# Performance work log

Measured on AMD Instinct MI355X. Metric: run time of the kernel, lower is better.

The kernel has to match this reference:

```python
import jax, jax.numpy as jnp
import numpy as np

N_NODES = 50000
N_EDGES = 600000  # incidence entries; hyperedge ids also live in [0, N_NODES)
HID = 128


def _prelu(x, a):
    return jnp.where(x >= 0, x, a * x)


def _hypergraph_conv(x, W, b, node_idx, edge_idx, num_nodes, num_hedges):
    # PyG HypergraphConv (use_attention=False, heads=1):
    # out = D^{-1} H B^{-1} H^T (X Theta) + bias
    xw = x @ W  # [N, F]
    ones = jnp.ones(node_idx.shape[0], dtype=x.dtype)
    D = jax.ops.segment_sum(ones, node_idx, num_segments=num_nodes)   # node degree
    B = jax.ops.segment_sum(ones, edge_idx, num_segments=num_hedges)  # hyperedge degree
    Dinv = jnp.where(D > 0, 1.0 / D, 0.0)
    Binv = jnp.where(B > 0, 1.0 / B, 0.0)
    # node -> hyperedge aggregation, scaled by B^{-1}
    m = jax.ops.segment_sum(xw[node_idx], edge_idx, num_segments=num_hedges) * Binv[:, None]
    # hyperedge -> node aggregation, scaled by D^{-1}
    out = jax.ops.segment_sum(m[edge_idx], node_idx, num_segments=num_nodes) * Dinv[:, None]
    return out + b


def setup_inputs() -> dict:
    key = jax.random.key(0)
    k1, k2, k3, k4, k5 = jax.random.split(key, 5)
    x = jax.random.normal(k1, (N_NODES, HID), dtype=jnp.float32)
    hyper_edge_index = jax.random.randint(k2, (2, N_EDGES), 0, N_NODES, dtype=jnp.int64)
    # kaiming-normal-ish linear weights, zero biases (per init_weights)
    std = float(np.sqrt(2.0 / HID))
    W1 = jax.random.normal(k3, (HID, HID), dtype=jnp.float32) * std
    W2 = jax.random.normal(k4, (HID, HID), dtype=jnp.float32) * std
    b1 = jnp.zeros((HID,), dtype=jnp.float32)
    b2 = jnp.zeros((HID,), dtype=jnp.float32)
    prelu_a = jnp.full((1,), 0.25, dtype=jnp.float32)  # nn.PReLU default
    return {"x": x, "hyper_edge_index": hyper_edge_index,
            "W1": W1, "b1": b1, "W2": W2, "b2": b2, "prelu_a": prelu_a}


def reference(x, hyper_edge_index, W1, b1, W2, b2, prelu_a):
    node_idx = hyper_edge_index[0]
    edge_idx = hyper_edge_index[1]
    h = _hypergraph_conv(x, W1, b1, node_idx, edge_idx, N_NODES, N_NODES)
    h = _prelu(h, prelu_a)
    h = _hypergraph_conv(h, W2, b2, node_idx, edge_idx, N_NODES, N_NODES)
    h = h + x  # residual
    return _prelu(h, prelu_a)
```

## Files before the change

kernel.cpp:

```cpp
#include <hip/hip_runtime.h>

typedef unsigned short u16;
typedef unsigned int   u32;
typedef unsigned long long u64;

#define HID 128
#define KPB 512
#define NBMAX 256
#define IPB 4096
#define CAP 12288

typedef __bf16 bf16x8 __attribute__((ext_vector_type(8)));
typedef float  f32x4  __attribute__((ext_vector_type(4)));

__device__ inline float u2f(u32 u){ union{u32 u;float f;} v; v.u=u; return v.f; }
__device__ inline u32   f2u(float f){ union{float f;u32 u;} v; v.f=f; return v.u; }
__device__ inline u32  f2bfu(float f){ u32 b=f2u(f); return ((b + 0x7FFFu + ((b>>16)&1u))>>16)&0xFFFFu; }
__device__ inline float blo(u32 u){ return u2f(u<<16); }
__device__ inline float bhi(u32 u){ return u2f(u & 0xFFFF0000u); }
__device__ inline u32  pk(float lo, float hi){ return (f2bfu(hi)<<16) | f2bfu(lo); }

__global__ __launch_bounds__(256) void k_f2bf4(const float4* __restrict__ in, ushort4* __restrict__ out, int n4){
    int i = blockIdx.x*256 + threadIdx.x;
    if (i < n4){
        float4 v = in[i];
        ushort4 o;
        o.x = (u16)f2bfu(v.x); o.y = (u16)f2bfu(v.y);
        o.z = (u16)f2bfu(v.z); o.w = (u16)f2bfu(v.w);
        out[i] = o;
    }
}

__global__ __launch_bounds__(256) void k_wfrag(const float* __restrict__ W, u16* __restrict__ Wf){
    int id = blockIdx.x*256 + threadIdx.x;
    int i = id & 7, l = (id>>3)&63, j = (id>>9)&7, s = id>>12;
    int k = s*32 + ((l>>4)<<3) + i;
    int n = (j<<4) + (l&15);
    Wf[id] = (u16)f2bfu(W[k*HID + n]);
}

__global__ __launch_bounds__(256) void k_hist(const int* __restrict__ nidx, const int* __restrict__ eidx,
                                              int* __restrict__ hist, int nE, int nN, int nb){
    __shared__ int h[NBMAX];
    for (int t=threadIdx.x; t<nb; t+=256) h[t]=0;
    __syncthreads();
    int base = blockIdx.x*IPB;
    for (int k=threadIdx.x; k<IPB; k+=256){
        int j = base+k;
        if (j < nE){
            int n = nidx[j], e = eidx[j];
            atomicAdd(&h[n>>9], 1);
            atomicAdd(&h[(nN+e)>>9], 1);
        }
    }
    __syncthreads();
    for (int t=threadIdx.x; t<nb; t+=256) if (h[t]) atomicAdd(&hist[t], h[t]);
}

__global__ __launch_bounds__(256) void k_bscan(const int* __restrict__ hist, int* __restrict__ bbase,
                                               int* __restrict__ bfill, int* __restrict__ off,
                                               int nb, int nkeys, int total){
    __shared__ int sd[256];
    int t = threadIdx.x;
    int v = (t < nb) ? hist[t] : 0;
    sd[t] = v; __syncthreads();
    for (int o=1;o<256;o<<=1){ int u = (t>=o)? sd[t-o] : 0; __syncthreads(); sd[t]+=u; __syncthreads(); }
    int ex = sd[t] - v;
    if (t < nb){ bbase[t] = ex; bfill[t] = ex; }
    if (t == 0){ bbase[nb] = total; off[nkeys] = total; }
}

__global__ __launch_bounds__(256) void k_part(const int* __restrict__ nidx, const int* __restrict__ eidx,
                                              int* __restrict__ bfill, u64* __restrict__ pairs,
                                              int nE, int nN, int nb){
    __shared__ int h[NBMAX], rsv[NBMAX], fl[NBMAX];
    for (int t=threadIdx.x; t<nb; t+=256){ h[t]=0; fl[t]=0; }
    __syncthreads();
    int base = blockIdx.x*IPB;
    for (int k=threadIdx.x; k<IPB; k+=256){
        int j = base+k;
        if (j < nE){
            int n = nidx[j], e = eidx[j];
            atomicAdd(&h[n>>9], 1);
            atomicAdd(&h[(nN+e)>>9], 1);
        }
    }
    __syncthreads();
    for (int t=threadIdx.x; t<nb; t+=256){ if (h[t]) rsv[t] = atomicAdd(&bfill[t], h[t]); }
    __syncthreads();
    for (int k=threadIdx.x; k<IPB; k+=256){
        int j = base+k;
        if (j < nE){
            int n = nidx[j], e = eidx[j];
            int b1 = n>>9;
            int p1 = rsv[b1] + atomicAdd(&fl[b1], 1);
            pairs[p1] = ((u64)(u32)n << 32) | (u32)e;
            int k2 = nN + e;
            int b2 = k2>>9;
            int p2 = rsv[b2] + atomicAdd(&fl[b2], 1);
            pairs[p2] = ((u64)(u32)k2 << 32) | (u32)n;
        }
    }
}

__global__ __launch_bounds__(256) void k_bucket(const u64* __restrict__ pairs, const int* __restrict__ bbase,
                                                int* __restrict__ csr, int* __restrict__ off, int nkeys){
    __shared__ int cntS[KPB];
    __shared__ int fillS[KPB];
    __shared__ int sd[256];
    __shared__ int vals[CAP];
    int b = blockIdx.x;
    int t = threadIdx.x;
    int base = bbase[b];
    int n = bbase[b+1] - base;
    int k0 = b * KPB;

    for (int i=t; i<KPB; i+=256) cntS[i] = 0;
    __syncthreads();
    for (int i=t; i<n; i+=256){
        u64 p = pairs[base+i];
        int kl = (int)(p>>32) - k0;
        atomicAdd(&cntS[kl], 1);
    }
    __syncthreads();
    int c0 = cntS[2*t], c1 = cntS[2*t+1];
    int s = c0 + c1;
    sd[t] = s; __syncthreads();
    for (int o=1;o<256;o<<=1){ int u = (t>=o)? sd[t-o] : 0; __syncthreads(); sd[t]+=u; __syncthreads(); }
    int ex = sd[t] - s;
    __syncthreads();
    cntS[2*t]   = ex;        cntS[2*t+1]   = ex + c0;
    fillS[2*t]  = ex;        fillS[2*t+1]  = ex + c0;
    __syncthreads();
    for (int i=t; i<KPB; i+=256){
        int k = k0 + i;
        if (k < nkeys) off[k] = base + cntS[i];
    }
    bool fits = (n <= CAP);
    for (int i=t; i<n; i+=256){
        u64 p = pairs[base+i];
        int kl = (int)(p>>32) - k0;
        int pos = atomicAdd(&fillS[kl], 1);
        if (fits) vals[pos] = (int)(u32)p;
        else      csr[base+pos] = (int)(u32)p;
    }
    __syncthreads();
    if (fits){
        for (int i=t; i<n; i+=256) csr[base+i] = vals[i];
    }
}

__global__ __launch_bounds__(256) void k_gemm(const u16* __restrict__ A, const u16* __restrict__ Wf,
                                              u16* __restrict__ C, int M){
    int wave = blockIdx.x*4 + (threadIdx.x>>6);
    int lane = threadIdx.x & 63;
    int rtiles = M >> 4;
    if (wave >= rtiles) return;
    int row0 = wave << 4;

    const u16* Arow = A + (size_t)(row0 + (lane&15))*HID + ((lane>>4)<<3);
    const bf16x8* Wp = reinterpret_cast<const bf16x8*>(Wf) + lane;

    f32x4 acc[8];
    #pragma unroll
    for (int j=0;j<8;++j) acc[j] = (f32x4){0.f,0.f,0.f,0.f};

    #pragma unroll
    for (int s=0;s<4;++s){
        bf16x8 a = *reinterpret_cast<const bf16x8*>(Arow + s*32);
        #pragma unroll
        for (int j=0;j<8;++j){
            bf16x8 b = Wp[(s*8 + j)*64];
            acc[j] = __builtin_amdgcn_mfma_f32_16x16x32_bf16(a, b, acc[j], 0, 0, 0);
        }
    }
    int r0 = row0 + ((lane>>4)<<2);
    int c0 = lane & 15;
    #pragma unroll
    for (int j=0;j<8;++j){
        #pragma unroll
        for (int r=0;r<4;++r){
            C[(size_t)(r0+r)*HID + j*16 + c0] = (u16)f2bfu(acc[j][r]);
        }
    }
}

template<int MODE>
__global__ __launch_bounds__(256) void k_agg(const u32* __restrict__ tab, const int* __restrict__ csr,
                                             const int* __restrict__ off, void* __restrict__ outp,
                                             const float* __restrict__ bias, const float* __restrict__ resid,
                                             const float* __restrict__ aptr, int nrows){
    int d = blockIdx.x*4 + (threadIdx.x>>6);
    if (d >= nrows) return;
    int lane = threadIdx.x & 63;
    int g = lane >> 4;
    int c = lane & 15;
    int start = off[d], end = off[d+1];
    int deg = end - start;

    int myc = 0;
    if (lane < deg) myc = csr[start + lane];

    float a0=0.f,a1=0.f,a2=0.f,a3=0.f,a4=0.f,a5=0.f,a6=0.f,a7=0.f;
    int nb4 = deg < 64 ? deg : 64;
    for (int jb = 0; jb < nb4; jb += 4){
        int j = jb + g;
        int src = __shfl(myc, j, 64);
        uint4 v = make_uint4(0u,0u,0u,0u);
        if (j < nb4) v = *reinterpret_cast<const uint4*>(tab + (size_t)src*64 + (c<<2));
        a0 += blo(v.x); a1 += bhi(v.x);
        a2 += blo(v.y); a3 += bhi(v.y);
        a4 += blo(v.z); a5 += bhi(v.z);
        a6 += blo(v.w); a7 += bhi(v.w);
    }
    for (int j = start + 64; j < end; ++j){
        uint4 v = make_uint4(0u,0u,0u,0u);
        if (g == 0){
            int src = csr[j];
            v = *reinterpret_cast<const uint4*>(tab + (size_t)src*64 + (c<<2));
        }
        a0 += blo(v.x); a1 += bhi(v.x);
        a2 += blo(v.y); a3 += bhi(v.y);
        a4 += blo(v.z); a5 += bhi(v.z);
        a6 += blo(v.w); a7 += bhi(v.w);
    }
    a0 += __shfl_xor(a0,16,64); a0 += __shfl_xor(a0,32,64);
    a1 += __shfl_xor(a1,16,64); a1 += __shfl_xor(a1,32,64);
    a2 += __shfl_xor(a2,16,64); a2 += __shfl_xor(a2,32,64);
    a3 += __shfl_xor(a3,16,64); a3 += __shfl_xor(a3,32,64);
    a4 += __shfl_xor(a4,16,64); a4 += __shfl_xor(a4,32,64);
    a5 += __shfl_xor(a5,16,64); a5 += __shfl_xor(a5,32,64);
    a6 += __shfl_xor(a6,16,64); a6 += __shfl_xor(a6,32,64);
    a7 += __shfl_xor(a7,16,64); a7 += __shfl_xor(a7,32,64);

    if (g == 0){
        float s = (deg > 0) ? 1.0f/(float)deg : 0.f;
        a0*=s; a1*=s; a2*=s; a3*=s; a4*=s; a5*=s; a6*=s; a7*=s;
        if constexpr (MODE >= 1){
            float4 b0 = *reinterpret_cast<const float4*>(bias + (c<<3));
            float4 b1v = *reinterpret_cast<const float4*>(bias + (c<<3) + 4);
            a0+=b0.x; a1+=b0.y; a2+=b0.z; a3+=b0.w;
            a4+=b1v.x; a5+=b1v.y; a6+=b1v.z; a7+=b1v.w;
        }
        if constexpr (MODE == 2){
            const float* rp = resid + (size_t)d*HID + (c<<3);
            float4 r0 = *reinterpret_cast<const float4*>(rp);
            float4 r1 = *reinterpret_cast<const float4*>(rp + 4);
            a0+=r0.x; a1+=r0.y; a2+=r0.z; a3+=r0.w;
            a4+=r1.x; a5+=r1.y; a6+=r1.z; a7+=r1.w;
        }
        if constexpr (MODE >= 1){
            float al = aptr[0];
            a0 = (a0>=0.f)? a0 : al*a0;  a1 = (a1>=0.f)? a1 : al*a1;
            a2 = (a2>=0.f)? a2 : al*a2;  a3 = (a3>=0.f)? a3 : al*a3;
            a4 = (a4>=0.f)? a4 : al*a4;  a5 = (a5>=0.f)? a5 : al*a5;
            a6 = (a6>=0.f)? a6 : al*a6;  a7 = (a7>=0.f)? a7 : al*a7;
        }
        if constexpr (MODE == 2){
            float* op = (float*)outp + (size_t)d*HID + (c<<3);
            *reinterpret_cast<float4*>(op)     = make_float4(a0,a1,a2,a3);
            *reinterpret_cast<float4*>(op + 4) = make_float4(a4,a5,a6,a7);
        } else {
            uint4 wv;
            wv.x = pk(a0,a1); wv.y = pk(a2,a3); wv.z = pk(a4,a5); wv.w = pk(a6,a7);
            *reinterpret_cast<uint4*>((u32*)outp + (size_t)d*64 + (c<<2)) = wv;
        }
    }
}

extern "C" void kernel_launch(void* const* d_in, const int* in_sizes, int n_in,
                              void* d_out, int out_size, void* d_ws, size_t ws_size,
                              hipStream_t stream){
    (void)n_in; (void)out_size; (void)ws_size;
    const float* x  = (const float*)d_in[0];
    const int*  hei = (const int*)  d_in[1];
    const float* W1 = (const float*)d_in[2];
    const float* b1 = (const float*)d_in[3];
    const float* W2 = (const float*)d_in[4];
    const float* b2 = (const float*)d_in[5];
    const float* ap = (const float*)d_in[6];

    const int nN = in_sizes[0] / HID;
    const int nE = in_sizes[1] / 2;
    const int* nidx = hei;
    const int* eidx = hei + nE;
    const int nkeys = 2*nN;
    const int nb    = (nkeys + KPB - 1) / KPB;

    char* w = (char*)d_ws;
    size_t o = 0;
    auto alloc = [&](size_t bytes)->void*{
        void* p = (void*)(w + o);
        o += (bytes + 255) & ~(size_t)255;
        return p;
    };
    int* hist  = (int*)alloc((size_t)NBMAX*sizeof(int));
    int* bbase = (int*)alloc((size_t)(NBMAX+1)*sizeof(int));
    int* bfill = (int*)alloc((size_t)NBMAX*sizeof(int));
    int* off   = (int*)alloc(((size_t)nkeys+1)*sizeof(int));
    int* csr   = (int*)alloc((size_t)2*nE*sizeof(int));
    u64* pairs = (u64*)alloc((size_t)2*nE*sizeof(u64));
    u16* xb    = (u16*)alloc((size_t)nN*HID*sizeof(u16));
    u16* bufB  = (u16*)alloc((size_t)nN*HID*sizeof(u16));
    u16* bufC  = (u16*)alloc((size_t)nN*HID*sizeof(u16));
    u16* w1f   = (u16*)alloc((size_t)HID*HID*sizeof(u16));
    u16* w2f   = (u16*)alloc((size_t)HID*HID*sizeof(u16));

    hipMemsetAsync(hist, 0, (size_t)nb*sizeof(int), stream);

    const int n4 = nN*HID/4;
    k_f2bf4<<<(n4+255)/256, 256, 0, stream>>>((const float4*)x, (ushort4*)xb, n4);
    k_wfrag<<<64, 256, 0, stream>>>(W1, w1f);
    k_wfrag<<<64, 256, 0, stream>>>(W2, w2f);

    const int pgrid = (nE + IPB - 1)/IPB;
    k_hist <<<pgrid, 256, 0, stream>>>(nidx, eidx, hist, nE, nN, nb);
    k_bscan<<<1,     256, 0, stream>>>(hist, bbase, bfill, off, nb, nkeys, 2*nE);
    k_part <<<pgrid, 256, 0, stream>>>(nidx, eidx, bfill, pairs, nE, nN, nb);
    k_bucket<<<nb,   256, 0, stream>>>(pairs, bbase, csr, off, nkeys);

    const int rtiles = nN/16;
    const int ggrid  = (rtiles + 3)/4;
    const int agrid  = (nN + 3)/4;

    k_gemm<<<ggrid, 256, 0, stream>>>(xb, w1f, bufB, nN);
    k_agg<0><<<agrid, 256, 0, stream>>>((const u32*)bufB, csr, off + nN, bufC, nullptr, nullptr, nullptr, nN);
    k_agg<1><<<agrid, 256, 0, stream>>>((const u32*)bufC, csr, off,      xb,   b1, nullptr, ap, nN);
    k_gemm<<<ggrid, 256, 0, stream>>>(xb, w2f, bufB, nN);
    k_agg<0><<<agrid, 256, 0, stream>>>((const u32*)bufB, csr, off + nN, bufC, nullptr, nullptr, nullptr, nN);
    k_agg<2><<<agrid, 256, 0, stream>>>((const u32*)bufC, csr, off, d_out, b2, x, ap, nN);
}
```

Baseline: 258.7 us.

## Fuse input bf16 conversion into first GEMM, merge weight prep, halve bucket size

The separate fp32-to-bf16 conversion kernel for x is removed, and the first GEMM now reads fp32 x and converts in registers, avoiding a full write and re-read of a bf16 copy. The two weight-fragment kernels are merged into one launch. The CSR bucketing uses 256 keys per bucket instead of 512, which doubles the bucket count and halves per-block shared memory, and it simplifies the bucket scan to one key per thread. The first GEMM reads twice as many bytes of x, and the partition kernels get more, smaller blocks.

New measurement: 253.2 us. 2.1% less time.

```diff
diff --git a/kernel.cpp b/kernel.cpp
--- a/kernel.cpp
+++ b/kernel.cpp
@@ -5,10 +5,10 @@
 typedef unsigned long long u64;
 
 #define HID 128
-#define KPB 512
-#define NBMAX 256
-#define IPB 4096
-#define CAP 12288
+#define KPB 256
+#define NBMAX 512
+#define IPB 2048
+#define CAP 6144
 
 typedef __bf16 bf16x8 __attribute__((ext_vector_type(8)));
 typedef float  f32x4  __attribute__((ext_vector_type(4)));
@@ -20,19 +20,12 @@
 __device__ inline float bhi(u32 u){ return u2f(u & 0xFFFF0000u); }
 __device__ inline u32  pk(float lo, float hi){ return (f2bfu(hi)<<16) | f2bfu(lo); }
 
-__global__ __launch_bounds__(256) void k_f2bf4(const float4* __restrict__ in, ushort4* __restrict__ out, int n4){
-    int i = blockIdx.x*256 + threadIdx.x;
-    if (i < n4){
-        float4 v = in[i];
-        ushort4 o;
-        o.x = (u16)f2bfu(v.x); o.y = (u16)f2bfu(v.y);
-        o.z = (u16)f2bfu(v.z); o.w = (u16)f2bfu(v.w);
-        out[i] = o;
-    }
-}
-
-__global__ __launch_bounds__(256) void k_wfrag(const float* __restrict__ W, u16* __restrict__ Wf){
-    int id = blockIdx.x*256 + threadIdx.x;
+__global__ __launch_bounds__(256) void k_wfrag2(const float* __restrict__ W1, const float* __restrict__ W2,
+                                                u16* __restrict__ W1f, u16* __restrict__ W2f){
+    int gid = blockIdx.x*256 + threadIdx.x;
+    const float* W = (gid < 16384) ? W1 : W2;
+    u16* Wf = (gid < 16384) ? W1f : W2f;
+    int id = gid & 16383;
     int i = id & 7, l = (id>>3)&63, j = (id>>9)&7, s = id>>12;
     int k = s*32 + ((l>>4)<<3) + i;
     int n = (j<<4) + (l&15);
@@ -49,8 +42,8 @@
         int j = base+k;
         if (j < nE){
             int n = nidx[j], e = eidx[j];
-            atomicAdd(&h[n>>9], 1);
-            atomicAdd(&h[(nN+e)>>9], 1);
+            atomicAdd(&h[n>>8], 1);
+            atomicAdd(&h[(nN+e)>>8], 1);
         }
     }
     __syncthreads();
@@ -62,11 +55,14 @@
                                                int nb, int nkeys, int total){
     __shared__ int sd[256];
     int t = threadIdx.x;
-    int v = (t < nb) ? hist[t] : 0;
-    sd[t] = v; __syncthreads();
+    int c0 = (2*t   < nb) ? hist[2*t]   : 0;
+    int c1 = (2*t+1 < nb) ? hist[2*t+1] : 0;
+    int s = c0 + c1;
+    sd[t] = s; __syncthreads();
     for (int o=1;o<256;o<<=1){ int u = (t>=o)? sd[t-o] : 0; __syncthreads(); sd[t]+=u; __syncthreads(); }
-    int ex = sd[t] - v;
-    if (t < nb){ bbase[t] = ex; bfill[t] = ex; }
+    int ex = sd[t] - s;
+    if (2*t   < nb){ bbase[2*t]   = ex;      bfill[2*t]   = ex; }
+    if (2*t+1 < nb){ bbase[2*t+1] = ex+c0;   bfill[2*t+1] = ex+c0; }
     if (t == 0){ bbase[nb] = total; off[nkeys] = total; }
 }
 
@@ -81,8 +77,8 @@
         int j = base+k;
         if (j < nE){
             int n = nidx[j], e = eidx[j];
-            atomicAdd(&h[n>>9], 1);
-            atomicAdd(&h[(nN+e)>>9], 1);
+            atomicAdd(&h[n>>8], 1);
+            atomicAdd(&h[(nN+e)>>8], 1);
         }
     }
     __syncthreads();
@@ -92,11 +88,11 @@
         int j = base+k;
         if (j < nE){
             int n = nidx[j], e = eidx[j];
-            int b1 = n>>9;
+            int b1 = n>>8;
             int p1 = rsv[b1] + atomicAdd(&fl[b1], 1);
             pairs[p1] = ((u64)(u32)n << 32) | (u32)e;
             int k2 = nN + e;
-            int b2 = k2>>9;
+            int b2 = k2>>8;
             int p2 = rsv[b2] + atomicAdd(&fl[b2], 1);
             pairs[p2] = ((u64)(u32)k2 << 32) | (u32)n;
         }
@@ -107,7 +103,6 @@
                                                 int* __restrict__ csr, int* __restrict__ off, int nkeys){
     __shared__ int cntS[KPB];
     __shared__ int fillS[KPB];
-    __shared__ int sd[256];
     __shared__ int vals[CAP];
     int b = blockIdx.x;
     int t = threadIdx.x;
@@ -115,7 +110,7 @@
     int n = bbase[b+1] - base;
     int k0 = b * KPB;
 
-    for (int i=t; i<KPB; i+=256) cntS[i] = 0;
+    cntS[t] = 0;
     __syncthreads();
     for (int i=t; i<n; i+=256){
         u64 p = pairs[base+i];
@@ -123,19 +118,16 @@
         atomicAdd(&cntS[kl], 1);
     }
     __syncthreads();
-    int c0 = cntS[2*t], c1 = cntS[2*t+1];
-    int s = c0 + c1;
-    sd[t] = s; __syncthreads();
-    for (int o=1;o<256;o<<=1){ int u = (t>=o)? sd[t-o] : 0; __syncthreads(); sd[t]+=u; __syncthreads(); }
-    int ex = sd[t] - s;
-    __syncthreads();
-    cntS[2*t]   = ex;        cntS[2*t+1]   = ex + c0;
-    fillS[2*t]  = ex;        fillS[2*t+1]  = ex + c0;
-    __syncthreads();
-    for (int i=t; i<KPB; i+=256){
-        int k = k0 + i;
-        if (k < nkeys) off[k] = base + cntS[i];
-    }
+    int c = cntS[t];
+    __syncthreads();
+    fillS[t] = c; __syncthreads();
+    for (int o=1;o<256;o<<=1){ int u = (t>=o)? fillS[t-o] : 0; __syncthreads(); fillS[t]+=u; __syncthreads(); }
+    int ex = fillS[t] - c;
+    __syncthreads();
+    cntS[t] = ex; fillS[t] = ex;
+    __syncthreads();
+    int k = k0 + t;
+    if (k < nkeys) off[k] = base + ex;
     bool fits = (n <= CAP);
     for (int i=t; i<n; i+=256){
         u64 p = pairs[base+i];
@@ -172,6 +164,45 @@
         for (int j=0;j<8;++j){
             bf16x8 b = Wp[(s*8 + j)*64];
             acc[j] = __builtin_amdgcn_mfma_f32_16x16x32_bf16(a, b, acc[j], 0, 0, 0);
+        }
+    }
+    int r0 = row0 + ((lane>>4)<<2);
+    int c0 = lane & 15;
+    #pragma unroll
+    for (int j=0;j<8;++j){
+        #pragma unroll
+        for (int r=0;r<4;++r){
+            C[(size_t)(r0+r)*HID + j*16 + c0] = (u16)f2bfu(acc[j][r]);
+        }
+    }
+}
+
+__global__ __launch_bounds__(256) void k_gemm_f32(const float* __restrict__ A, const u16* __restrict__ Wf,
+                                                  u16* __restrict__ C, int M){
+    int wave = blockIdx.x*4 + (threadIdx.x>>6);
+    int lane = threadIdx.x & 63;
+    int rtiles = M >> 4;
+    if (wave >= rtiles) return;
+    int row0 = wave << 4;
+
+    const float* Arow = A + (size_t)(row0 + (lane&15))*HID + ((lane>>4)<<3);
+    const bf16x8* Wp = reinterpret_cast<const bf16x8*>(Wf) + lane;
+
+    f32x4 acc[8];
+    #pragma unroll
+    for (int j=0;j<8;++j) acc[j] = (f32x4){0.f,0.f,0.f,0.f};
+
+    #pragma unroll
+    for (int s=0;s<4;++s){
+        float4 f0 = *reinterpret_cast<const float4*>(Arow + s*32);
+        float4 f1 = *reinterpret_cast<const float4*>(Arow + s*32 + 4);
+        union { u16 h[8]; bf16x8 v; } au;
+        au.h[0]=(u16)f2bfu(f0.x); au.h[1]=(u16)f2bfu(f0.y); au.h[2]=(u16)f2bfu(f0.z); au.h[3]=(u16)f2bfu(f0.w);
+        au.h[4]=(u16)f2bfu(f1.x); au.h[5]=(u16)f2bfu(f1.y); au.h[6]=(u16)f2bfu(f1.z); au.h[7]=(u16)f2bfu(f1.w);
+        #pragma unroll
+        for (int j=0;j<8;++j){
+            bf16x8 b = Wp[(s*8 + j)*64];
+            acc[j] = __builtin_amdgcn_mfma_f32_16x16x32_bf16(au.v, b, acc[j], 0, 0, 0);
         }
     }
     int r0 = row0 + ((lane>>4)<<2);
@@ -300,7 +331,7 @@
     int* off   = (int*)alloc(((size_t)nkeys+1)*sizeof(int));
     int* csr   = (int*)alloc((size_t)2*nE*sizeof(int));
     u64* pairs = (u64*)alloc((size_t)2*nE*sizeof(u64));
-    u16* xb    = (u16*)alloc((size_t)nN*HID*sizeof(u16));
+    u16* hb    = (u16*)alloc((size_t)nN*HID*sizeof(u16));
     u16* bufB  = (u16*)alloc((size_t)nN*HID*sizeof(u16));
     u16* bufC  = (u16*)alloc((size_t)nN*HID*sizeof(u16));
     u16* w1f   = (u16*)alloc((size_t)HID*HID*sizeof(u16));
@@ -308,10 +339,11 @@
 
     hipMemsetAsync(hist, 0, (size_t)nb*sizeof(int), stream);
 
-    const int n4 = nN*HID/4;
-    k_f2bf4<<<(n4+255)/256, 256, 0, stream>>>((const float4*)x, (ushort4*)xb, n4);
-    k_wfrag<<<64, 256, 0, stream>>>(W1, w1f);
-    k_wfrag<<<64, 256, 0, stream>>>(W2, w2f);
+    k_wfrag2<<<128, 256, 0, stream>>>(W1, W2, w1f, w2f);
+
+    const int rtiles = nN/16;
+    const int ggrid  = (rtiles + 3)/4;
+    k_gemm_f32<<<ggrid, 256, 0, stream>>>(x, w1f, bufB, nN);
 
     const int pgrid = (nE + IPB - 1)/IPB;
     k_hist <<<pgrid, 256, 0, stream>>>(nidx, eidx, hist, nE, nN, nb);
@@ -319,14 +351,11 @@
     k_part <<<pgrid, 256, 0, stream>>>(nidx, eidx, bfill, pairs, nE, nN, nb);
     k_bucket<<<nb,   256, 0, stream>>>(pairs, bbase, csr, off, nkeys);
 
-    const int rtiles = nN/16;
-    const int ggrid  = (rtiles + 3)/4;
     const int agrid  = (nN + 3)/4;
 
-    k_gemm<<<ggrid, 256, 0, stream>>>(xb, w1f, bufB, nN);
     k_agg<0><<<agrid, 256, 0, stream>>>((const u32*)bufB, csr, off + nN, bufC, nullptr, nullptr, nullptr, nN);
-    k_agg<1><<<agrid, 256, 0, stream>>>((const u32*)bufC, csr, off,      xb,   b1, nullptr, ap, nN);
-    k_gemm<<<ggrid, 256, 0, stream>>>(xb, w2f, bufB, nN);
+    k_agg<1><<<agrid, 256, 0, stream>>>((const u32*)bufC, csr, off,      hb,   b1, nullptr, ap, nN);
+    k_gemm<<<ggrid, 256, 0, stream>>>(hb, w2f, bufB, nN);
     k_agg<0><<<agrid, 256, 0, stream>>>((const u32*)bufB, csr, off + nN, bufC, nullptr, nullptr, nullptr, nN);
     k_agg<2><<<agrid, 256, 0, stream>>>((const u32*)bufC, csr, off, d_out, b2, x, ap, nN);
 }
```
